# Performance work log

Hardware: AMD Instinct MI355X
Metric: run time of the kernel (lower is better)

Reference implementation:

```python
import jax, jax.numpy as jnp
import numpy as np

B, T, C = 2, 2048, 1024
H = 16
HS = C // H  # 64
LN_EPS = 1e-5

def setup_inputs() -> dict:
    key = jax.random.key(0)
    ks = jax.random.split(key, 12)
    s = lambda *sh: 0.02
    inp = {
        'x': jax.random.normal(ks[0], (B, T, C), jnp.float32),
        # per-head Q/K/V weights (bias=False), stacked over heads: [H, C, HS]
        'wq': jax.random.normal(ks[1], (H, C, HS), jnp.float32) * 0.02,
        'wk': jax.random.normal(ks[2], (H, C, HS), jnp.float32) * 0.02,
        'wv': jax.random.normal(ks[3], (H, C, HS), jnp.float32) * 0.02,
        'w_proj': jax.random.normal(ks[4], (C, C), jnp.float32) * 0.02,
        'b_proj': jnp.zeros((C,), jnp.float32),
        'w1': jax.random.normal(ks[5], (C, 4 * C), jnp.float32) * 0.02,
        'b1': jnp.zeros((4 * C,), jnp.float32),
        'w2': jax.random.normal(ks[6], (4 * C, C), jnp.float32) * 0.02,
        'b2': jnp.zeros((C,), jnp.float32),
        'ln1_g': jnp.ones((C,), jnp.float32),
        'ln1_b': jnp.zeros((C,), jnp.float32),
        'ln2_g': jnp.ones((C,), jnp.float32),
        'ln2_b': jnp.zeros((C,), jnp.float32),
    }
    return inp

def _layernorm(x, g, b):
    mu = jnp.mean(x, axis=-1, keepdims=True)
    var = jnp.mean(jnp.square(x - mu), axis=-1, keepdims=True)
    return (x - mu) * jax.lax.rsqrt(var + LN_EPS) * g + b

def reference(x, wq, wk, wv, w_proj, b_proj, w1, b1, w2, b2, ln1_g, ln1_b, ln2_g, ln2_b):
    Bx, Tx, Cx = x.shape
    h = _layernorm(x, ln1_g, ln1_b)
    q = jnp.einsum('btc,hcd->bhtd', h, wq)
    k = jnp.einsum('btc,hcd->bhtd', h, wk)
    v = jnp.einsum('btc,hcd->bhtd', h, wv)
    # NOTE: original scales by n_embedding**-0.5 (C), not head_size**-0.5
    scores = jnp.einsum('bhtd,bhsd->bhts', q, k) * (Cx ** -0.5)
    causal = jnp.tril(jnp.ones((Tx, Tx), bool))
    scores = jnp.where(causal, scores, -jnp.inf)
    att = jax.nn.softmax(scores, axis=-1)  # [B,H,T,T]
    out = jnp.einsum('bhts,bhsd->bhtd', att, v)
    out = out.transpose(0, 2, 1, 3).reshape(Bx, Tx, Cx)  # concat heads
    out = out @ w_proj + b_proj
    x = x + out
    h2 = _layernorm(x, ln2_g, ln2_b)
    ff = jax.nn.relu(h2 @ w1 + b1) @ w2 + b2
    return x + ff
```

## Files before the change

kernel.cpp:

```cpp
#include <hip/hip_runtime.h>
#include <hip/hip_bf16.h>
#include <stdint.h>

typedef __bf16 bf16_t;
typedef __bf16 bf16x8 __attribute__((ext_vector_type(8)));
typedef __bf16 bf16x4 __attribute__((ext_vector_type(4)));
typedef float f32x4 __attribute__((ext_vector_type(4)));

static constexpr int TT = 2048, CC = 1024;

__device__ __forceinline__ void gld_lds16(const void* g, void* l) {
  __builtin_amdgcn_global_load_lds((const __attribute__((address_space(1))) void*)g,
                                   (__attribute__((address_space(3))) void*)l, 16, 0, 0);
}

__global__ __launch_bounds__(256) void transpose_cvt(const float* __restrict__ in,
                                                     bf16_t* __restrict__ out,
                                                     int K, int N) {
  __shared__ float t[32][33];
  const int k0 = blockIdx.x * 32, n0 = blockIdx.y * 32;
  const size_t boff = (size_t)blockIdx.z * K * N;
  in += boff;
  out += boff;
  const int tx = threadIdx.x & 31, ty = threadIdx.x >> 5;
#pragma unroll
  for (int j = 0; j < 4; ++j)
    t[ty + j * 8][tx] = in[(size_t)(k0 + ty + j * 8) * N + n0 + tx];
  __syncthreads();
#pragma unroll
  for (int j = 0; j < 4; ++j)
    out[(size_t)(n0 + ty + j * 8) * K + k0 + tx] = (bf16_t)t[tx][ty + j * 8];
}

__global__ __launch_bounds__(256) void ln_f32_bf16(const float* __restrict__ x,
                                                   const float* __restrict__ g,
                                                   const float* __restrict__ b,
                                                   bf16_t* __restrict__ out) {
  const int row = blockIdx.x;
  const int tid = threadIdx.x;
  const float4 v = ((const float4*)(x + (size_t)row * CC))[tid];
  float s = v.x + v.y + v.z + v.w;
  float q = v.x * v.x + v.y * v.y + v.z * v.z + v.w * v.w;
#pragma unroll
  for (int off = 1; off < 64; off <<= 1) {
    s += __shfl_xor(s, off);
    q += __shfl_xor(q, off);
  }
  __shared__ float red[8];
  const int wave = tid >> 6, lane = tid & 63;
  if (lane == 0) { red[wave] = s; red[4 + wave] = q; }
  __syncthreads();
  s = red[0] + red[1] + red[2] + red[3];
  q = red[4] + red[5] + red[6] + red[7];
  const float mu = s * (1.0f / CC);
  float var = q * (1.0f / CC) - mu * mu;
  var = fmaxf(var, 0.f);
  const float rstd = rsqrtf(var + 1e-5f);
  const float4 gv = ((const float4*)g)[tid];
  const float4 bv = ((const float4*)b)[tid];
  bf16x4 o;
  o[0] = (bf16_t)((v.x - mu) * rstd * gv.x + bv.x);
  o[1] = (bf16_t)((v.y - mu) * rstd * gv.y + bv.y);
  o[2] = (bf16_t)((v.z - mu) * rstd * gv.z + bv.z);
  o[3] = (bf16_t)((v.w - mu) * rstd * gv.w + bv.w);
  *(bf16x4*)(out + (size_t)row * CC + tid * 4) = o;
}

template <int EPI, int BN>
__global__ __launch_bounds__(256) void gemm_bt(const bf16_t* __restrict__ A,
                                               const bf16_t* __restrict__ Bt,
                                               void* __restrict__ Cout,
                                               const float* __restrict__ bias,
                                               const float* __restrict__ res,
                                               bf16_t* __restrict__ vt,
                                               int M, int N, int K) {
  constexpr int WN = BN / 2;
  constexpr int NF = BN / 32;
  constexpr int NB = BN / 32;
  __shared__ alignas(16) bf16_t As[128 * 64];
  __shared__ alignas(16) bf16_t Bs[BN * 64];
  const int tid = threadIdx.x;
  const int wave = tid >> 6, lane = tid & 63;
  const int lr = lane & 15, lg = lane >> 4;
  const int wm = wave >> 1, wn = wave & 1;
  const int tm0 = blockIdx.y * 128, tn0 = blockIdx.x * BN;

  const int sr = lane >> 3;
  const int scs = (lane & 7) ^ sr;
  const bf16_t* Ag[4];
#pragma unroll
  for (int i = 0; i < 4; ++i)
    Ag[i] = A + (size_t)(tm0 + i * 32 + wave * 8 + sr) * K + scs * 8;
  const bf16_t* Bg[NB];
#pragma unroll
  for (int i = 0; i < NB; ++i)
    Bg[i] = Bt + (size_t)(tn0 + i * 32 + wave * 8 + sr) * K + scs * 8;

  f32x4 acc[4][NF] = {};
  for (int k0 = 0; k0 < K; k0 += 64) {
#pragma unroll
    for (int i = 0; i < 4; ++i)
      gld_lds16(Ag[i] + k0, As + (i * 32 + wave * 8) * 64);
#pragma unroll
    for (int i = 0; i < NB; ++i)
      gld_lds16(Bg[i] + k0, Bs + (i * 32 + wave * 8) * 64);
    __syncthreads();
    bf16x8 af[2][4], bfr[2][NF];
#pragma unroll
    for (int kk = 0; kk < 2; ++kk) {
      const int ch = ((kk * 4 + lg) ^ (lr & 7)) * 8;
#pragma unroll
      for (int m = 0; m < 4; ++m)
        af[kk][m] = *(const bf16x8*)&As[(wm * 64 + m * 16 + lr) * 64 + ch];
#pragma unroll
      for (int n = 0; n < NF; ++n)
        bfr[kk][n] = *(const bf16x8*)&Bs[(wn * WN + n * 16 + lr) * 64 + ch];
    }
#pragma unroll
    for (int kk = 0; kk < 2; ++kk)
#pragma unroll
      for (int m = 0; m < 4; ++m)
#pragma unroll
        for (int n = 0; n < NF; ++n)
          acc[m][n] =
              __builtin_amdgcn_mfma_f32_16x16x32_bf16(af[kk][m], bfr[kk][n], acc[m][n], 0, 0, 0);
    __syncthreads();
  }
#pragma unroll
  for (int m = 0; m < 4; ++m) {
#pragma unroll
    for (int i = 0; i < 4; ++i) {
      const int row = tm0 + wm * 64 + m * 16 + lg * 4 + i;
#pragma unroll
      for (int n = 0; n < NF; ++n) {
        const int col = tn0 + wn * WN + n * 16 + lr;
        float v = acc[m][n][i];
        if (EPI == 1) v = fmaxf(v + bias[col], 0.f);
        if (EPI == 2) v = v + bias[col] + res[(size_t)row * N + col];
        if (EPI == 2) {
          ((float*)Cout)[(size_t)row * N + col] = v;
        } else if (EPI == 3) {
          if (col >= 2048) {
            const int hd = col - 2048;
            const size_t vidx =
                ((size_t)((row >> 11) * 16 + (hd >> 6)) * 64 + (hd & 63)) * TT + (row & (TT - 1));
            vt[vidx] = (bf16_t)v;
          } else {
            ((bf16_t*)Cout)[(size_t)row * N + col] = (bf16_t)v;
          }
        } else {
          ((bf16_t*)Cout)[(size_t)row * N + col] = (bf16_t)v;
        }
      }
    }
  }
}

__global__ __launch_bounds__(256, 3) void attn_fwd(const bf16_t* __restrict__ qkv,
                                                   const bf16_t* __restrict__ Vt,
                                                   bf16_t* __restrict__ O) {
  const int bh = blockIdx.x;
  const int bb = bh >> 4, hh = bh & 15;
  const int qt = 31 - (int)blockIdx.y;
  const int qbase = qt * 64;
  const int tid = threadIdx.x;
  const int wave = tid >> 6, lane = tid & 63;
  const int lr = lane & 15, lg = lane >> 4;
  const bf16_t* Qp = qkv + (size_t)bb * TT * 3072 + hh * 64;
  const bf16_t* Kp = Qp + 1024;
  const bf16_t* Vh = Vt + (size_t)bh * 64 * TT;

  constexpr int KLP = 72;
  constexpr int VLP = 136;
  constexpr int PLP = 136;
  __shared__ alignas(16) bf16_t Klds[128 * KLP];
  __shared__ alignas(16) bf16_t Vlds[64 * VLP];
  __shared__ alignas(16) bf16_t PlS[4][16 * PLP];
  bf16_t* Pw = PlS[wave];

  const int ksr = wave * 32 + (lane >> 3);
  const int ksc = (lane & 7) * 8;
  const int vsr = wave * 16 + (lane >> 4);
  const int vsc = (lane & 15) * 8;

  const int qrow = qbase + wave * 16;
  bf16x8 qf0, qf1;
  {
    const bf16x8 a = *(const bf16x8*)(Qp + (size_t)(qrow + lr) * 3072 + lg * 8);
    const bf16x8 b = *(const bf16x8*)(Qp + (size_t)(qrow + lr) * 3072 + 32 + lg * 8);
#pragma unroll
    for (int j = 0; j < 8; ++j) {
      qf0[j] = (bf16_t)((float)a[j] * 0.03125f);
      qf1[j] = (bf16_t)((float)b[j] * 0.03125f);
    }
  }

  f32x4 oacc[4] = {};
  float m_r[4], l_r[4];
#pragma unroll
  for (int i = 0; i < 4; ++i) { m_r[i] = -1e38f; l_r[i] = 0.f; }

  bf16x8 kpre[4], vpre[4];
#pragma unroll
  for (int i = 0; i < 4; ++i) {
    kpre[i] = *(const bf16x8*)(Kp + (size_t)(ksr + i * 8) * 3072 + ksc);
    vpre[i] = *(const bf16x8*)(Vh + (size_t)(vsr + i * 4) * TT + vsc);
  }
#pragma unroll
  for (int i = 0; i < 4; ++i) {
    *(bf16x8*)&Klds[(ksr + i * 8) * KLP + ksc] = kpre[i];
    *(bf16x8*)&Vlds[(vsr + i * 4) * VLP + vsc] = vpre[i];
  }
  __syncthreads();

  const int nt = (qt >> 1) + 1;
  for (int t = 0; t < nt; ++t) {
    const int s0 = t * 128;
    const int sn = (t + 1 < nt) ? s0 + 128 : s0;
#pragma unroll
    for (int i = 0; i < 4; ++i) {
      kpre[i] = *(const bf16x8*)(Kp + (size_t)(sn + ksr + i * 8) * 3072 + ksc);
      vpre[i] = *(const bf16x8*)(Vh + (size_t)(vsr + i * 4) * TT + sn + vsc);
    }

    const int u = (qrow - s0) >> 4;
    const int cmc = min(u | 1, 7);

    float P[8][4];
    __builtin_amdgcn_s_setprio(1);
#pragma unroll
    for (int ct = 0; ct < 8; ++ct) {
      if (ct <= cmc) {
        const bf16x8 kf0 = *(const bf16x8*)&Klds[(ct * 16 + lr) * KLP + lg * 8];
        const bf16x8 kf1 = *(const bf16x8*)&Klds[(ct * 16 + lr) * KLP + 32 + lg * 8];
        f32x4 z = {};
        z = __builtin_amdgcn_mfma_f32_16x16x32_bf16(qf0, kf0, z, 0, 0, 0);
        z = __builtin_amdgcn_mfma_f32_16x16x32_bf16(qf1, kf1, z, 0, 0, 0);
        if (ct >= u) {
          const int sg = s0 + ct * 16 + lr;
#pragma unroll
          for (int i = 0; i < 4; ++i)
            P[ct][i] = (sg > qrow + lg * 4 + i) ? -1e30f : z[i];
        } else {
#pragma unroll
          for (int i = 0; i < 4; ++i) P[ct][i] = z[i];
        }
      } else {
#pragma unroll
        for (int i = 0; i < 4; ++i) P[ct][i] = -1e30f;
      }
    }
    __builtin_amdgcn_s_setprio(0);

    float lmax[4];
#pragma unroll
    for (int i = 0; i < 4; ++i) {
      float m0 = fmaxf(fmaxf(P[0][i], P[1][i]), fmaxf(P[2][i], P[3][i]));
      float m1 = fmaxf(fmaxf(P[4][i], P[5][i]), fmaxf(P[6][i], P[7][i]));
      lmax[i] = fmaxf(m0, m1);
    }
    const bool ok = (lmax[0] <= m_r[0] + 8.f) && (lmax[1] <= m_r[1] + 8.f) &&
                    (lmax[2] <= m_r[2] + 8.f) && (lmax[3] <= m_r[3] + 8.f);
    if (!__all(ok)) {
      float rm[4] = {lmax[0], lmax[1], lmax[2], lmax[3]};
#pragma unroll
      for (int off = 1; off < 16; off <<= 1)
#pragma unroll
        for (int i = 0; i < 4; ++i) rm[i] = fmaxf(rm[i], __shfl_xor(rm[i], off));
#pragma unroll
      for (int i = 0; i < 4; ++i) {
        const float mn = fmaxf(m_r[i], rm[i]);
        const float alpha = __expf(m_r[i] - mn);
        m_r[i] = mn;
        l_r[i] *= alpha;
#pragma unroll
        for (int db = 0; db < 4; ++db) oacc[db][i] *= alpha;
      }
    }

#pragma unroll
    for (int i = 0; i < 4; ++i) {
      float ls = 0.f;
#pragma unroll
      for (int ct = 0; ct < 8; ++ct) {
        const float p = __expf(P[ct][i] - m_r[i]);
        P[ct][i] = p;
        ls += p;
      }
      l_r[i] += ls;
    }

#pragma unroll
    for (int ct = 0; ct < 8; ++ct) {
      if (ct <= cmc) {
#pragma unroll
        for (int i = 0; i < 4; ++i) {
          const int q = lg * 4 + i;
          const int col = (ct * 16 + lr) ^ ((lg >> 1) << 4);
          Pw[q * PLP + col] = (bf16_t)P[ct][i];
        }
      }
    }
    asm volatile("s_waitcnt lgkmcnt(0)" ::: "memory");
    __builtin_amdgcn_sched_barrier(0);

    const int kcm = cmc >> 1;
    __builtin_amdgcn_s_setprio(1);
#pragma unroll
    for (int kc = 0; kc < 4; ++kc) {
      if (kc <= kcm) {
        const bf16x8 pf =
            *(const bf16x8*)&Pw[lr * PLP + ((kc * 32 + lg * 8) ^ ((lr >> 3) << 4))];
#pragma unroll
        for (int db = 0; db < 4; ++db) {
          const bf16x8 vf = *(const bf16x8*)&Vlds[(db * 16 + lr) * VLP + kc * 32 + lg * 8];
          oacc[db] = __builtin_amdgcn_mfma_f32_16x16x32_bf16(pf, vf, oacc[db], 0, 0, 0);
        }
      }
    }
    __builtin_amdgcn_s_setprio(0);

    if (t + 1 < nt) {
      __syncthreads();
#pragma unroll
      for (int i = 0; i < 4; ++i) {
        *(bf16x8*)&Klds[(ksr + i * 8) * KLP + ksc] = kpre[i];
        *(bf16x8*)&Vlds[(vsr + i * 4) * VLP + vsc] = vpre[i];
      }
      __syncthreads();
    }
  }

#pragma unroll
  for (int off = 1; off < 16; off <<= 1)
#pragma unroll
    for (int i = 0; i < 4; ++i) l_r[i] += __shfl_xor(l_r[i], off);

  bf16_t* Op = O + ((size_t)bb * TT + qrow) * CC + hh * 64;
#pragma unroll
  for (int i = 0; i < 4; ++i) {
    const float rl = 1.0f / l_r[i];
#pragma unroll
    for (int db = 0; db < 4; ++db)
      Op[(size_t)(lg * 4 + i) * CC + db * 16 + lr] = (bf16_t)(oacc[db][i] * rl);
  }
}

extern "C" void kernel_launch(void* const* d_in, const int* in_sizes, int n_in,
                              void* d_out, int out_size, void* d_ws, size_t ws_size,
                              hipStream_t stream) {
  const float* x      = (const float*)d_in[0];
  const float* wq     = (const float*)d_in[1];
  const float* wk     = (const float*)d_in[2];
  const float* wv     = (const float*)d_in[3];
  const float* w_proj = (const float*)d_in[4];
  const float* b_proj = (const float*)d_in[5];
  const float* w1     = (const float*)d_in[6];
  const float* b1     = (const float*)d_in[7];
  const float* w2     = (const float*)d_in[8];
  const float* b2     = (const float*)d_in[9];
  const float* ln1_g  = (const float*)d_in[10];
  const float* ln1_b  = (const float*)d_in[11];
  const float* ln2_g  = (const float*)d_in[12];
  const float* ln2_b  = (const float*)d_in[13];

  char* ws = (char*)d_ws;
  const size_t MB = 1024 * 1024;
  bf16_t* h1    = (bf16_t*)(ws + 0);
  bf16_t* Bqkv  = (bf16_t*)(ws + 8 * MB);
  bf16_t* Bproj = (bf16_t*)(ws + 14 * MB);
  bf16_t* B1w   = (bf16_t*)(ws + 16 * MB);
  bf16_t* B2w   = (bf16_t*)(ws + 24 * MB);
  bf16_t* qkv   = (bf16_t*)(ws + 32 * MB);
  bf16_t* Obuf  = (bf16_t*)(ws + 56 * MB);
  float*  res1  = (float*)(ws + 64 * MB);
  bf16_t* Vt    = (bf16_t*)(ws + 64 * MB);
  bf16_t* h2    = (bf16_t*)(ws + 80 * MB);
  bf16_t* a1    = (bf16_t*)(ws + 32 * MB);
  float*  outp  = (float*)d_out;

  dim3 blk(256);
  transpose_cvt<<<dim3(32, 2, 16), blk, 0, stream>>>(wq, Bqkv, 1024, 64);
  transpose_cvt<<<dim3(32, 2, 16), blk, 0, stream>>>(wk, Bqkv + 1024 * 1024, 1024, 64);
  transpose_cvt<<<dim3(32, 2, 16), blk, 0, stream>>>(wv, Bqkv + 2 * 1024 * 1024, 1024, 64);
  transpose_cvt<<<dim3(32, 32, 1), blk, 0, stream>>>(w_proj, Bproj, 1024, 1024);
  transpose_cvt<<<dim3(32, 128, 1), blk, 0, stream>>>(w1, B1w, 1024, 4096);
  transpose_cvt<<<dim3(128, 32, 1), blk, 0, stream>>>(w2, B2w, 4096, 1024);

  ln_f32_bf16<<<dim3(4096), blk, 0, stream>>>(x, ln1_g, ln1_b, h1);
  gemm_bt<3, 128><<<dim3(24, 32), blk, 0, stream>>>(h1, Bqkv, qkv, nullptr, nullptr, Vt,
                                                    4096, 3072, 1024);
  attn_fwd<<<dim3(32, 32), blk, 0, stream>>>(qkv, Vt, Obuf);
  gemm_bt<2, 64><<<dim3(16, 32), blk, 0, stream>>>(Obuf, Bproj, res1, b_proj, x, nullptr,
                                                   4096, 1024, 1024);
  ln_f32_bf16<<<dim3(4096), blk, 0, stream>>>(res1, ln2_g, ln2_b, h2);
  gemm_bt<1, 128><<<dim3(32, 32), blk, 0, stream>>>(h2, B1w, a1, b1, nullptr, nullptr,
                                                    4096, 4096, 1024);
  gemm_bt<2, 64><<<dim3(16, 32), blk, 0, stream>>>(a1, B2w, outp, b2, res1, nullptr,
                                                   4096, 1024, 4096);
}
```

Before: 269.6 us.

## Double-buffer LDS tiles in bf16 GEMM to overlap global loads with MFMA

The GEMM kernel now keeps two LDS buffers for the A and B tiles. It issues the direct-to-LDS global loads for the next K tile before computing on the current one, and uses a single barrier per iteration with explicit vmcnt/lgkmcnt waits. It also raises wave priority around the MFMA block. The aim is to hide global memory latency behind matrix math, at the cost of twice the LDS per block, which may lower occupancy.

```diff
diff --git a/kernel.cpp b/kernel.cpp
--- a/kernel.cpp
+++ b/kernel.cpp
@@ -77,8 +77,8 @@
   constexpr int WN = BN / 2;
   constexpr int NF = BN / 32;
   constexpr int NB = BN / 32;
-  __shared__ alignas(16) bf16_t As[128 * 64];
-  __shared__ alignas(16) bf16_t Bs[BN * 64];
+  __shared__ alignas(16) bf16_t As[2][128 * 64];
+  __shared__ alignas(16) bf16_t Bs[2][BN * 64];
   const int tid = threadIdx.x;
   const int wave = tid >> 6, lane = tid & 63;
   const int lr = lane & 15, lg = lane >> 4;
@@ -96,26 +96,42 @@
   for (int i = 0; i < NB; ++i)
     Bg[i] = Bt + (size_t)(tn0 + i * 32 + wave * 8 + sr) * K + scs * 8;
 
+  auto STAGE = [&](int k0, bf16_t* Ad, bf16_t* Bd) {
+#pragma unroll
+    for (int i = 0; i < 4; ++i)
+      gld_lds16(Ag[i] + k0, Ad + (i * 32 + wave * 8) * 64);
+#pragma unroll
+    for (int i = 0; i < NB; ++i)
+      gld_lds16(Bg[i] + k0, Bd + (i * 32 + wave * 8) * 64);
+  };
+
   f32x4 acc[4][NF] = {};
-  for (int k0 = 0; k0 < K; k0 += 64) {
-#pragma unroll
-    for (int i = 0; i < 4; ++i)
-      gld_lds16(Ag[i] + k0, As + (i * 32 + wave * 8) * 64);
-#pragma unroll
-    for (int i = 0; i < NB; ++i)
-      gld_lds16(Bg[i] + k0, Bs + (i * 32 + wave * 8) * 64);
-    __syncthreads();
+  const int NT = K >> 6;
+
+  STAGE(0, As[0], Bs[0]);
+  asm volatile("s_waitcnt vmcnt(0)" ::: "memory");
+  __builtin_amdgcn_s_barrier();
+
+  for (int t = 0; t < NT; ++t) {
+    const int cur = t & 1;
+    bf16_t* Ac = As[cur];
+    bf16_t* Bc = Bs[cur];
+    if (t + 1 < NT) STAGE((t + 1) << 6, As[cur ^ 1], Bs[cur ^ 1]);
+
     bf16x8 af[2][4], bfr[2][NF];
 #pragma unroll
     for (int kk = 0; kk < 2; ++kk) {
       const int ch = ((kk * 4 + lg) ^ (lr & 7)) * 8;
 #pragma unroll
       for (int m = 0; m < 4; ++m)
-        af[kk][m] = *(const bf16x8*)&As[(wm * 64 + m * 16 + lr) * 64 + ch];
+        af[kk][m] = *(const bf16x8*)&Ac[(wm * 64 + m * 16 + lr) * 64 + ch];
 #pragma unroll
       for (int n = 0; n < NF; ++n)
-        bfr[kk][n] = *(const bf16x8*)&Bs[(wn * WN + n * 16 + lr) * 64 + ch];
-    }
+        bfr[kk][n] = *(const bf16x8*)&Bc[(wn * WN + n * 16 + lr) * 64 + ch];
+    }
+    asm volatile("s_waitcnt lgkmcnt(0)" ::: "memory");
+    __builtin_amdgcn_sched_barrier(0);
+    __builtin_amdgcn_s_setprio(1);
 #pragma unroll
     for (int kk = 0; kk < 2; ++kk)
 #pragma unroll
@@ -124,8 +140,12 @@
         for (int n = 0; n < NF; ++n)
           acc[m][n] =
               __builtin_amdgcn_mfma_f32_16x16x32_bf16(af[kk][m], bfr[kk][n], acc[m][n], 0, 0, 0);
-    __syncthreads();
-  }
+    __builtin_amdgcn_s_setprio(0);
+    asm volatile("s_waitcnt vmcnt(0)" ::: "memory");
+    __builtin_amdgcn_sched_barrier(0);
+    __builtin_amdgcn_s_barrier();
+  }
+
 #pragma unroll
   for (int m = 0; m < 4; ++m) {
 #pragma unroll
```

After: 256.6 us. 1.05x faster.
